# Performance work log

Measured on AMD Instinct MI355X. Metric: run time of the kernel, lower is better.

The kernel has to match this reference:

```python
import jax, jax.numpy as jnp
import numpy as np

DIM = 768
NUM_HEADS = 12
HEAD_DIM = DIM // NUM_HEADS
SCALE = HEAD_DIM ** -0.5


def setup_inputs() -> dict:
    key = jax.random.key(0)
    ks = jax.random.split(key, 6)
    B, N, C = 4, 2048, DIM
    x = jax.random.normal(ks[0], (B, N, C), dtype=jnp.float32)
    qkv_weight = jax.random.normal(ks[1], (3 * C, C), dtype=jnp.float32) * (C ** -0.5)
    q_bias = jax.random.normal(ks[2], (C,), dtype=jnp.float32) * 0.02
    v_bias = jax.random.normal(ks[3], (C,), dtype=jnp.float32) * 0.02
    proj_weight = jax.random.normal(ks[4], (C, C), dtype=jnp.float32) * (C ** -0.5)
    proj_bias = jax.random.normal(ks[5], (C,), dtype=jnp.float32) * 0.02
    return {"x": x, "qkv_weight": qkv_weight, "q_bias": q_bias,
            "v_bias": v_bias, "proj_weight": proj_weight, "proj_bias": proj_bias}


def reference(x, qkv_weight, q_bias, v_bias, proj_weight, proj_bias):
    B, N, C = x.shape
    # bias = concat(q_bias, zeros_like(v_bias), v_bias)
    bias = jnp.concatenate([q_bias, jnp.zeros_like(v_bias), v_bias])
    qkv = x @ qkv_weight.T + bias                      # [B, N, 3C]
    qkv = qkv.reshape(B, N, 3, NUM_HEADS, HEAD_DIM)
    q, k, v = jnp.moveaxis(qkv, 2, 0)                  # each [B, N, H, hd]
    q = jnp.transpose(q, (0, 2, 1, 3)) * SCALE         # [B, H, N, hd]
    k = jnp.transpose(k, (0, 2, 1, 3))
    v = jnp.transpose(v, (0, 2, 1, 3))
    attn = jax.nn.softmax(jnp.einsum('bhqd,bhkd->bhqk', q, k), axis=-1)
    out = jnp.einsum('bhqk,bhkd->bhqd', attn, v)       # [B, H, N, hd]
    out = jnp.transpose(out, (0, 2, 1, 3)).reshape(B, N, C)
    return out @ proj_weight.T + proj_bias
```

## Files before the change

kernel.cpp:

```cpp
#include <hip/hip_runtime.h>
#include <cstdint>
#include <cstddef>

typedef _Float16 f16;
typedef _Float16 f16x8 __attribute__((ext_vector_type(8)));
typedef _Float16 f16x4 __attribute__((ext_vector_type(4)));
typedef __fp16 h16x2 __attribute__((ext_vector_type(2)));
typedef float f32x4 __attribute__((ext_vector_type(4)));

#define DIM 768
#define NHEAD 12
#define HD 64
#define BATCH 4
#define SEQ 2048
#define MROWS (BATCH*SEQ)
#define C3 (3*DIM)
#define NBH (BATCH*NHEAD)

__device__ __forceinline__ f32x4 mfma32(f16x8 a, f16x8 b, f32x4 c) {
  return __builtin_amdgcn_mfma_f32_16x16x32_f16(a, b, c, 0, 0, 0);
}
__device__ __forceinline__ f32x4 mfma16(f16x4 a, f16x4 b, f32x4 c) {
  return __builtin_amdgcn_mfma_f32_16x16x16f16(a, b, c, 0, 0, 0);
}

__device__ __forceinline__ void gl2lds16(const void* g, void* l) {
  __builtin_amdgcn_global_load_lds(
      (const __attribute__((address_space(1))) void*)g,
      (__attribute__((address_space(3))) void*)l, 16, 0, 0);
}

__global__ __launch_bounds__(256) void k_convert(
    const float* __restrict__ x, const float* __restrict__ wqkv,
    const float* __restrict__ wproj,
    f16* __restrict__ xh, f16* __restrict__ wqh, f16* __restrict__ wph)
{
  const int NX = MROWS*DIM/4, NW = C3*DIM/4;
  int i = blockIdx.x * 256 + threadIdx.x;
  const float4* src; f16* dst; int idx;
  if (i < NX)         { src = (const float4*)x;     dst = xh;  idx = i; }
  else if (i < NX+NW) { src = (const float4*)wqkv;  dst = wqh; idx = i - NX; }
  else                { src = (const float4*)wproj; dst = wph; idx = i - NX - NW; }
  float4 v = src[idx];
  union { f16 h[4]; uint64_t u; } r;
  r.h[0] = (f16)v.x; r.h[1] = (f16)v.y; r.h[2] = (f16)v.z; r.h[3] = (f16)v.w;
  ((uint64_t*)dst)[idx] = r.u;
}

__device__ __forceinline__ void gemm_tile(
    const f16* __restrict__ A, const f16* __restrict__ B,
    int lda, int ldb, int K, int am0, int bn0,
    f16* smem, f32x4 acc[4][4])
{
  f16* sA0 = smem;         f16* sA1 = smem + 4096;
  f16* sB0 = smem + 8192;  f16* sB1 = smem + 12288;
  const int tid = threadIdx.x, wid = tid >> 6;
  const int lane = tid & 63, lane15 = lane & 15, quad = lane >> 4;
  const int wm = wid >> 1, wn = wid & 1;

  auto stage = [&](int k0, f16* sA, f16* sB) {
    #pragma unroll
    for (int i = 0; i < 2; i++) {
      int j = i*256 + tid;
      int row = j >> 2;
      int sc  = (j & 3) ^ ((row >> 1) & 3);
      gl2lds16(A + (size_t)(am0 + row)*lda + k0 + sc*8, sA + (i*256 + wid*64)*8);
      gl2lds16(B + (size_t)(bn0 + row)*ldb + k0 + sc*8, sB + (i*256 + wid*64)*8);
    }
  };

  const int NK = K >> 5;
  stage(0, sA0, sB0);
  for (int kk = 0; kk < NK; kk++) {
    f16* cA = (kk & 1) ? sA1 : sA0;
    f16* cB = (kk & 1) ? sB1 : sB0;
    __syncthreads();
    if (kk + 1 < NK)
      stage((kk + 1) << 5, (kk & 1) ? sA0 : sA1, (kk & 1) ? sB0 : sB1);
    f16x8 af[4], bf[4];
    #pragma unroll
    for (int t = 0; t < 4; t++) {
      int ra = wm*64 + t*16 + lane15;
      af[t] = *(const f16x8*)(cA + ra*32 + ((quad ^ ((ra >> 1) & 3)) << 3));
      int rb = wn*64 + t*16 + lane15;
      bf[t] = *(const f16x8*)(cB + rb*32 + ((quad ^ ((rb >> 1) & 3)) << 3));
    }
    #pragma unroll
    for (int mt = 0; mt < 4; mt++)
      #pragma unroll
      for (int nt = 0; nt < 4; nt++)
        acc[mt][nt] = mfma32(af[mt], bf[nt], acc[mt][nt]);
  }
}

__global__ __launch_bounds__(256, 4) void k_qkv(
    const f16* __restrict__ xh, const f16* __restrict__ wqh,
    const float* __restrict__ q_bias, const float* __restrict__ v_bias,
    f16* __restrict__ Qh, f16* __restrict__ Kh, f16* __restrict__ Vt)
{
  __shared__ f16 smem[16384];
  f32x4 acc[4][4];
  const f32x4 z4 = {0.f, 0.f, 0.f, 0.f};
  #pragma unroll
  for (int a = 0; a < 4; a++)
    #pragma unroll
    for (int b = 0; b < 4; b++) acc[a][b] = z4;

  const int tid = threadIdx.x, wid = tid >> 6, lane = tid & 63;
  const int lane15 = lane & 15, quad = lane >> 4;
  const int wm = wid >> 1, wn = wid & 1;
  const int cblk = blockIdx.x * 128;
  const int mblk = blockIdx.y * 128;
  const int bb = mblk >> 11, nbase = mblk & (SEQ - 1);
  const float QS = 0.125f * 1.4426950408889634f;

  if (cblk < 2*DIM) {
    gemm_tile(wqh, xh, DIM, DIM, DIM, cblk, mblk, smem, acc);
    const bool isQ = (cblk < DIM);
    #pragma unroll
    for (int mt = 0; mt < 4; mt++) {
      int c0 = cblk + wm*64 + mt*16 + quad*4;
      int cr = isQ ? c0 : (c0 - DIM);
      int h = cr >> 6, d0 = cr & 63;
      float4 qb4 = isQ ? *(const float4*)(q_bias + c0) : make_float4(0,0,0,0);
      f16* dst = isQ ? Qh : Kh;
      f16* base = dst + (((size_t)(bb*NHEAD + h)*SEQ + nbase) << 6) + d0;
      #pragma unroll
      for (int nt = 0; nt < 4; nt++) {
        int n = wn*64 + nt*16 + lane15;
        f32x4 v = acc[mt][nt];
        f16x4 hv;
        if (isQ) {
          hv[0] = (f16)((v[0] + qb4.x) * QS); hv[1] = (f16)((v[1] + qb4.y) * QS);
          hv[2] = (f16)((v[2] + qb4.z) * QS); hv[3] = (f16)((v[3] + qb4.w) * QS);
        } else {
          hv[0] = (f16)v[0]; hv[1] = (f16)v[1]; hv[2] = (f16)v[2]; hv[3] = (f16)v[3];
        }
        *(f16x4*)(base + ((size_t)n << 6)) = hv;
      }
    }
  } else {
    gemm_tile(xh, wqh, DIM, DIM, DIM, mblk, cblk, smem, acc);
    #pragma unroll
    for (int nt = 0; nt < 4; nt++) {
      int c = cblk + wn*64 + nt*16 + lane15;
      int c2 = c - 2*DIM;
      int h = c2 >> 6, d = c2 & 63;
      float b = v_bias[c2];
      f16* base = Vt + ((size_t)(bb*NHEAD + h)*HD + d)*SEQ + nbase;
      #pragma unroll
      for (int mt = 0; mt < 4; mt++) {
        int n0 = wm*64 + mt*16 + quad*4;
        f32x4 v = acc[mt][nt];
        f16x4 hv = {(f16)(v[0]+b), (f16)(v[1]+b), (f16)(v[2]+b), (f16)(v[3]+b)};
        *(f16x4*)(base + n0) = hv;
      }
    }
  }
}

#define KVT 128
#define NIT (SEQ/KVT)
__global__ __launch_bounds__(256, 3) void k_attn(
    const f16* __restrict__ Qh, const f16* __restrict__ Kh,
    const f16* __restrict__ Vt, f16* __restrict__ attnh)
{
  __shared__ f16 smem[2*8192 + 64*132];
  f16* sK0 = smem;
  f16* sK1 = smem + 8192;
  f16* sV  = smem + 16384;

  const int tid = threadIdx.x, wid = tid >> 6, lane = tid & 63;
  const int lane15 = lane & 15, quad = lane >> 4;
  const int q0 = blockIdx.x * 128;
  const int bh = blockIdx.y;
  const int qw = q0 + wid*32;

  const f16* Kbh = Kh + (size_t)bh*SEQ*HD;
  const f16* Vbh = Vt + (size_t)bh*HD*SEQ;

  f16x8 qf[2][2];
  #pragma unroll
  for (int qt = 0; qt < 2; qt++)
    #pragma unroll
    for (int ks = 0; ks < 2; ks++)
      qf[qt][ks] = *(const f16x8*)(Qh + ((size_t)bh*SEQ + qw + qt*16 + lane15)*HD
                                      + ks*32 + quad*8);

  f32x4 o[4][2];
  f32x4 sacc[2];
  const f32x4 z4 = {0.f, 0.f, 0.f, 0.f};
  #pragma unroll
  for (int dt = 0; dt < 4; dt++)
    #pragma unroll
    for (int qt = 0; qt < 2; qt++) o[dt][qt] = z4;
  sacc[0] = z4; sacc[1] = z4;
  const f16x4 one4 = {(f16)1.f, (f16)1.f, (f16)1.f, (f16)1.f};

  const int vrow = tid >> 2, vcg = (tid & 3) * 32;
  const f16* vsrc = Vbh + (size_t)vrow*SEQ + vcg;

  auto stageK = [&](int kv0, f16* sK) {
    #pragma unroll
    for (int i = 0; i < 4; i++) {
      int j = i*256 + tid;
      int row = j >> 3;
      int sc  = (j & 7) ^ (row & 7);
      gl2lds16(Kbh + (size_t)(kv0 + row)*HD + sc*8, sK + (i*256 + wid*64)*8);
    }
  };

  stageK(0, sK0);
  f16x8 vreg[4];
  #pragma unroll
  for (int j = 0; j < 4; j++) vreg[j] = *(const f16x8*)(vsrc + j*8);

  for (int it = 0; it < NIT; it++) {
    f16* cK = (it & 1) ? sK1 : sK0;
    __syncthreads();
    #pragma unroll
    for (int j = 0; j < 4; j++) {
      union { f16x8 v; f16x4 h[2]; } u; u.v = vreg[j];
      *(f16x4*)(sV + vrow*132 + vcg + j*8)     = u.h[0];
      *(f16x4*)(sV + vrow*132 + vcg + j*8 + 4) = u.h[1];
    }
    __syncthreads();
    if (it + 1 < NIT) {
      stageK((it + 1)*KVT, (it & 1) ? sK0 : sK1);
      #pragma unroll
      for (int j = 0; j < 4; j++)
        vreg[j] = *(const f16x8*)(vsrc + (it + 1)*KVT + j*8);
    }

    #pragma unroll
    for (int c = 0; c < 4; c++) {
      f16x8 ka[2][2];
      #pragma unroll
      for (int kt = 0; kt < 2; kt++) {
        int rb = c*32 + kt*16 + lane15;
        #pragma unroll
        for (int ks = 0; ks < 2; ks++)
          ka[ks][kt] = *(const f16x8*)(cK + rb*64 + (((ks*4 + quad) ^ (rb & 7)) << 3));
      }
      f32x4 s[2][2];
      #pragma unroll
      for (int kt = 0; kt < 2; kt++)
        #pragma unroll
        for (int qt = 0; qt < 2; qt++) s[kt][qt] = z4;
      #pragma unroll
      for (int ks = 0; ks < 2; ks++)
        #pragma unroll
        for (int kt = 0; kt < 2; kt++)
          #pragma unroll
          for (int qt = 0; qt < 2; qt++)
            s[kt][qt] = mfma32(ka[ks][kt], qf[qt][ks], s[kt][qt]);

      f16x4 pb[2][2];
      #pragma unroll
      for (int kt = 0; kt < 2; kt++)
        #pragma unroll
        for (int qt = 0; qt < 2; qt++) {
          union { h16x2 g2[2]; f16x4 h4; } u;
          u.g2[0] = __builtin_amdgcn_cvt_pkrtz(exp2f(s[kt][qt][0]), exp2f(s[kt][qt][1]));
          u.g2[1] = __builtin_amdgcn_cvt_pkrtz(exp2f(s[kt][qt][2]), exp2f(s[kt][qt][3]));
          pb[kt][qt] = u.h4;
        }
      #pragma unroll
      for (int kt = 0; kt < 2; kt++)
        #pragma unroll
        for (int qt = 0; qt < 2; qt++)
          sacc[qt] = mfma16(one4, pb[kt][qt], sacc[qt]);

      #pragma unroll
      for (int dt = 0; dt < 4; dt++) {
        int row = dt*16 + lane15;
        #pragma unroll
        for (int kt = 0; kt < 2; kt++) {
          int c16 = 4*c + 2*kt + (quad >> 1);
          f16x4 va = *(const f16x4*)(sV + row*132 + c16*8 + (quad & 1)*4);
          #pragma unroll
          for (int qt = 0; qt < 2; qt++)
            o[dt][qt] = mfma16(va, pb[kt][qt], o[dt][qt]);
        }
      }
    }
  }

  float inv[2] = {1.f / sacc[0][0], 1.f / sacc[1][0]};

  __syncthreads();
  f16* tb = smem + wid * (32 * 72);
  #pragma unroll
  for (int dt = 0; dt < 4; dt++)
    #pragma unroll
    for (int qt = 0; qt < 2; qt++) {
      f32x4 v = o[dt][qt];
      float iv = inv[qt];
      f16x4 hx = {(f16)(v[0]*iv), (f16)(v[1]*iv), (f16)(v[2]*iv), (f16)(v[3]*iv)};
      *(f16x4*)(tb + (qt*16 + lane15)*72 + dt*16 + quad*4) = hx;
    }
  __syncthreads();
  const int b = bh / NHEAD, h = bh % NHEAD;
  #pragma unroll
  for (int i = 0; i < 4; i++) {
    int row = i*8 + (lane >> 3);
    f16x8 rv = *(const f16x8*)(tb + row*72 + (lane & 7)*8);
    *(f16x8*)(attnh + ((size_t)b*SEQ + qw + row)*DIM + h*HD + (lane & 7)*8) = rv;
  }
}

__global__ __launch_bounds__(256, 4) void k_proj(
    const f16* __restrict__ ah, const f16* __restrict__ wph,
    const float* __restrict__ pbias, float* __restrict__ out)
{
  __shared__ f16 smem[16384];
  f32x4 acc[4][4];
  const f32x4 z4 = {0.f, 0.f, 0.f, 0.f};
  #pragma unroll
  for (int a = 0; a < 4; a++)
    #pragma unroll
    for (int b = 0; b < 4; b++) acc[a][b] = z4;

  const int cblk = blockIdx.y * 128;
  const int mblk = blockIdx.x * 128;
  gemm_tile(wph, ah, DIM, DIM, DIM, cblk, mblk, smem, acc);

  const int tid = threadIdx.x, wid = tid >> 6, lane = tid & 63;
  const int lane15 = lane & 15, quad = lane >> 4;
  const int wm = wid >> 1, wn = wid & 1;
  #pragma unroll
  for (int mt = 0; mt < 4; mt++) {
    int c0 = cblk + wm*64 + mt*16 + quad*4;
    float4 b4 = *(const float4*)(pbias + c0);
    #pragma unroll
    for (int nt = 0; nt < 4; nt++) {
      int m = mblk + wn*64 + nt*16 + lane15;
      f32x4 v = acc[mt][nt];
      float4 r = make_float4(v[0]+b4.x, v[1]+b4.y, v[2]+b4.z, v[3]+b4.w);
      *(float4*)(out + (size_t)m*DIM + c0) = r;
    }
  }
}

extern "C" void kernel_launch(void* const* d_in, const int* in_sizes, int n_in,
                              void* d_out, int out_size, void* d_ws, size_t ws_size,
                              hipStream_t stream) {
  const float* x    = (const float*)d_in[0];
  const float* wqkv = (const float*)d_in[1];
  const float* qb   = (const float*)d_in[2];
  const float* vb   = (const float*)d_in[3];
  const float* wp   = (const float*)d_in[4];
  const float* pb   = (const float*)d_in[5];
  float* out = (float*)d_out;

  f16* p = (f16*)d_ws;
  f16* xh  = p; p += (size_t)MROWS*DIM;
  f16* wqh = p; p += (size_t)C3*DIM;
  f16* wph = p; p += (size_t)DIM*DIM;
  f16* Qh  = p; p += (size_t)NBH*SEQ*HD;
  f16* Kh  = p; p += (size_t)NBH*SEQ*HD;
  f16* Vt  = p; p += (size_t)NBH*SEQ*HD;
  f16* attnh = xh;

  k_convert<<<8448, 256, 0, stream>>>(x, wqkv, wp, xh, wqh, wph);
  k_qkv<<<dim3(C3/128, MROWS/128), 256, 0, stream>>>(xh, wqh, qb, vb, Qh, Kh, Vt);
  k_attn<<<dim3(SEQ/128, NBH), 256, 0, stream>>>(Qh, Kh, Vt, attnh);
  k_proj<<<dim3(MROWS/128, DIM/128), 256, 0, stream>>>(attnh, wph, pb, out);
}
```

Measured before the change: 235.5 us.

## Use 2-wave attention blocks with 64 queries per wave; shrink proj tile to 128x64

```diff
diff --git a/kernel.cpp b/kernel.cpp
--- a/kernel.cpp
+++ b/kernel.cpp
@@ -89,6 +89,57 @@
     for (int mt = 0; mt < 4; mt++)
       #pragma unroll
       for (int nt = 0; nt < 4; nt++)
+        acc[mt][nt] = mfma32(af[mt], bf[nt], acc[mt][nt]);
+  }
+}
+
+__device__ __forceinline__ void gemm_tile_128x64(
+    const f16* __restrict__ A, const f16* __restrict__ B,
+    int lda, int ldb, int K, int am0, int bn0,
+    f16* smem, f32x4 acc[4][2])
+{
+  f16* sA0 = smem;         f16* sA1 = smem + 4096;
+  f16* sB0 = smem + 8192;  f16* sB1 = smem + 10240;
+  const int tid = threadIdx.x, wid = tid >> 6;
+  const int lane = tid & 63, lane15 = lane & 15, quad = lane >> 4;
+  const int wm = wid >> 1, wn = wid & 1;
+
+  auto stage = [&](int k0, f16* sA, f16* sB) {
+    #pragma unroll
+    for (int i = 0; i < 2; i++) {
+      int j = i*256 + tid;
+      int row = j >> 2;
+      int sc  = (j & 3) ^ ((row >> 1) & 3);
+      gl2lds16(A + (size_t)(am0 + row)*lda + k0 + sc*8, sA + (i*256 + wid*64)*8);
+    }
+    int rowb = tid >> 2;
+    int scb  = (tid & 3) ^ ((rowb >> 1) & 3);
+    gl2lds16(B + (size_t)(bn0 + rowb)*ldb + k0 + scb*8, sB + (wid*64)*8);
+  };
+
+  const int NK = K >> 5;
+  stage(0, sA0, sB0);
+  for (int kk = 0; kk < NK; kk++) {
+    f16* cA = (kk & 1) ? sA1 : sA0;
+    f16* cB = (kk & 1) ? sB1 : sB0;
+    __syncthreads();
+    if (kk + 1 < NK)
+      stage((kk + 1) << 5, (kk & 1) ? sA0 : sA1, (kk & 1) ? sB0 : sB1);
+    f16x8 af[4], bf[2];
+    #pragma unroll
+    for (int t = 0; t < 4; t++) {
+      int ra = wm*64 + t*16 + lane15;
+      af[t] = *(const f16x8*)(cA + ra*32 + ((quad ^ ((ra >> 1) & 3)) << 3));
+    }
+    #pragma unroll
+    for (int t = 0; t < 2; t++) {
+      int rb = wn*32 + t*16 + lane15;
+      bf[t] = *(const f16x8*)(cB + rb*32 + ((quad ^ ((rb >> 1) & 3)) << 3));
+    }
+    #pragma unroll
+    for (int mt = 0; mt < 4; mt++)
+      #pragma unroll
+      for (int nt = 0; nt < 2; nt++)
         acc[mt][nt] = mfma32(af[mt], bf[nt], acc[mt][nt]);
   }
 }
@@ -161,7 +212,7 @@
 
 #define KVT 128
 #define NIT (SEQ/KVT)
-__global__ __launch_bounds__(256, 3) void k_attn(
+__global__ __launch_bounds__(128, 2) void k_attn(
     const f16* __restrict__ Qh, const f16* __restrict__ Kh,
     const f16* __restrict__ Vt, f16* __restrict__ attnh)
 {
@@ -174,52 +225,53 @@
   const int lane15 = lane & 15, quad = lane >> 4;
   const int q0 = blockIdx.x * 128;
   const int bh = blockIdx.y;
-  const int qw = q0 + wid*32;
+  const int qw = q0 + wid*64;
 
   const f16* Kbh = Kh + (size_t)bh*SEQ*HD;
   const f16* Vbh = Vt + (size_t)bh*HD*SEQ;
 
-  f16x8 qf[2][2];
-  #pragma unroll
-  for (int qt = 0; qt < 2; qt++)
+  f16x8 qf[4][2];
+  #pragma unroll
+  for (int qt = 0; qt < 4; qt++)
     #pragma unroll
     for (int ks = 0; ks < 2; ks++)
       qf[qt][ks] = *(const f16x8*)(Qh + ((size_t)bh*SEQ + qw + qt*16 + lane15)*HD
                                       + ks*32 + quad*8);
 
-  f32x4 o[4][2];
-  f32x4 sacc[2];
+  f32x4 o[4][4];
+  f32x4 sacc[4];
   const f32x4 z4 = {0.f, 0.f, 0.f, 0.f};
   #pragma unroll
   for (int dt = 0; dt < 4; dt++)
     #pragma unroll
-    for (int qt = 0; qt < 2; qt++) o[dt][qt] = z4;
-  sacc[0] = z4; sacc[1] = z4;
+    for (int qt = 0; qt < 4; qt++) o[dt][qt] = z4;
+  #pragma unroll
+  for (int qt = 0; qt < 4; qt++) sacc[qt] = z4;
   const f16x4 one4 = {(f16)1.f, (f16)1.f, (f16)1.f, (f16)1.f};
 
-  const int vrow = tid >> 2, vcg = (tid & 3) * 32;
+  const int vrow = tid >> 1, vcg = (tid & 1) * 64;
   const f16* vsrc = Vbh + (size_t)vrow*SEQ + vcg;
 
   auto stageK = [&](int kv0, f16* sK) {
     #pragma unroll
-    for (int i = 0; i < 4; i++) {
-      int j = i*256 + tid;
+    for (int i = 0; i < 8; i++) {
+      int j = i*128 + tid;
       int row = j >> 3;
       int sc  = (j & 7) ^ (row & 7);
-      gl2lds16(Kbh + (size_t)(kv0 + row)*HD + sc*8, sK + (i*256 + wid*64)*8);
+      gl2lds16(Kbh + (size_t)(kv0 + row)*HD + sc*8, sK + (i*128 + wid*64)*8);
     }
   };
 
   stageK(0, sK0);
-  f16x8 vreg[4];
-  #pragma unroll
-  for (int j = 0; j < 4; j++) vreg[j] = *(const f16x8*)(vsrc + j*8);
+  f16x8 vreg[8];
+  #pragma unroll
+  for (int j = 0; j < 8; j++) vreg[j] = *(const f16x8*)(vsrc + j*8);
 
   for (int it = 0; it < NIT; it++) {
     f16* cK = (it & 1) ? sK1 : sK0;
     __syncthreads();
     #pragma unroll
-    for (int j = 0; j < 4; j++) {
+    for (int j = 0; j < 8; j++) {
       union { f16x8 v; f16x4 h[2]; } u; u.v = vreg[j];
       *(f16x4*)(sV + vrow*132 + vcg + j*8)     = u.h[0];
       *(f16x4*)(sV + vrow*132 + vcg + j*8 + 4) = u.h[1];
@@ -228,7 +280,7 @@
     if (it + 1 < NIT) {
       stageK((it + 1)*KVT, (it & 1) ? sK0 : sK1);
       #pragma unroll
-      for (int j = 0; j < 4; j++)
+      for (int j = 0; j < 8; j++)
         vreg[j] = *(const f16x8*)(vsrc + (it + 1)*KVT + j*8);
     }
 
@@ -242,24 +294,24 @@
         for (int ks = 0; ks < 2; ks++)
           ka[ks][kt] = *(const f16x8*)(cK + rb*64 + (((ks*4 + quad) ^ (rb & 7)) << 3));
       }
-      f32x4 s[2][2];
+      f32x4 s[2][4];
       #pragma unroll
       for (int kt = 0; kt < 2; kt++)
         #pragma unroll
-        for (int qt = 0; qt < 2; qt++) s[kt][qt] = z4;
+        for (int qt = 0; qt < 4; qt++) s[kt][qt] = z4;
       #pragma unroll
       for (int ks = 0; ks < 2; ks++)
         #pragma unroll
         for (int kt = 0; kt < 2; kt++)
           #pragma unroll
-          for (int qt = 0; qt < 2; qt++)
+          for (int qt = 0; qt < 4; qt++)
             s[kt][qt] = mfma32(ka[ks][kt], qf[qt][ks], s[kt][qt]);
 
-      f16x4 pb[2][2];
+      f16x4 pb[2][4];
       #pragma unroll
       for (int kt = 0; kt < 2; kt++)
         #pragma unroll
-        for (int qt = 0; qt < 2; qt++) {
+        for (int qt = 0; qt < 4; qt++) {
           union { h16x2 g2[2]; f16x4 h4; } u;
           u.g2[0] = __builtin_amdgcn_cvt_pkrtz(exp2f(s[kt][qt][0]), exp2f(s[kt][qt][1]));
           u.g2[1] = __builtin_amdgcn_cvt_pkrtz(exp2f(s[kt][qt][2]), exp2f(s[kt][qt][3]));
@@ -268,7 +320,7 @@
       #pragma unroll
       for (int kt = 0; kt < 2; kt++)
         #pragma unroll
-        for (int qt = 0; qt < 2; qt++)
+        for (int qt = 0; qt < 4; qt++)
           sacc[qt] = mfma16(one4, pb[kt][qt], sacc[qt]);
 
       #pragma unroll
@@ -279,51 +331,52 @@
           int c16 = 4*c + 2*kt + (quad >> 1);
           f16x4 va = *(const f16x4*)(sV + row*132 + c16*8 + (quad & 1)*4);
           #pragma unroll
-          for (int qt = 0; qt < 2; qt++)
+          for (int qt = 0; qt < 4; qt++)
             o[dt][qt] = mfma16(va, pb[kt][qt], o[dt][qt]);
         }
       }
     }
   }
 
-  float inv[2] = {1.f / sacc[0][0], 1.f / sacc[1][0]};
+  float inv[4];
+  #pragma unroll
+  for (int qt = 0; qt < 4; qt++) inv[qt] = 1.f / sacc[qt][0];
 
   __syncthreads();
-  f16* tb = smem + wid * (32 * 72);
+  f16* tb = smem + wid * (64 * 72);
   #pragma unroll
   for (int dt = 0; dt < 4; dt++)
     #pragma unroll
-    for (int qt = 0; qt < 2; qt++) {
+    for (int qt = 0; qt < 4; qt++) {
       f32x4 v = o[dt][qt];
       float iv = inv[qt];
       f16x4 hx = {(f16)(v[0]*iv), (f16)(v[1]*iv), (f16)(v[2]*iv), (f16)(v[3]*iv)};
       *(f16x4*)(tb + (qt*16 + lane15)*72 + dt*16 + quad*4) = hx;
     }
-  __syncthreads();
   const int b = bh / NHEAD, h = bh % NHEAD;
   #pragma unroll
-  for (int i = 0; i < 4; i++) {
+  for (int i = 0; i < 8; i++) {
     int row = i*8 + (lane >> 3);
     f16x8 rv = *(const f16x8*)(tb + row*72 + (lane & 7)*8);
     *(f16x8*)(attnh + ((size_t)b*SEQ + qw + row)*DIM + h*HD + (lane & 7)*8) = rv;
   }
 }
 
-__global__ __launch_bounds__(256, 4) void k_proj(
+__global__ __launch_bounds__(256, 3) void k_proj(
     const f16* __restrict__ ah, const f16* __restrict__ wph,
     const float* __restrict__ pbias, float* __restrict__ out)
 {
-  __shared__ f16 smem[16384];
-  f32x4 acc[4][4];
+  __shared__ f16 smem[12288];
+  f32x4 acc[4][2];
   const f32x4 z4 = {0.f, 0.f, 0.f, 0.f};
   #pragma unroll
   for (int a = 0; a < 4; a++)
     #pragma unroll
-    for (int b = 0; b < 4; b++) acc[a][b] = z4;
+    for (int b = 0; b < 2; b++) acc[a][b] = z4;
 
   const int cblk = blockIdx.y * 128;
-  const int mblk = blockIdx.x * 128;
-  gemm_tile(wph, ah, DIM, DIM, DIM, cblk, mblk, smem, acc);
+  const int mblk = blockIdx.x * 64;
+  gemm_tile_128x64(wph, ah, DIM, DIM, DIM, cblk, mblk, smem, acc);
 
   const int tid = threadIdx.x, wid = tid >> 6, lane = tid & 63;
   const int lane15 = lane & 15, quad = lane >> 4;
@@ -333,8 +386,8 @@
     int c0 = cblk + wm*64 + mt*16 + quad*4;
     float4 b4 = *(const float4*)(pbias + c0);
     #pragma unroll
-    for (int nt = 0; nt < 4; nt++) {
-      int m = mblk + wn*64 + nt*16 + lane15;
+    for (int nt = 0; nt < 2; nt++) {
+      int m = mblk + wn*32 + nt*16 + lane15;
       f32x4 v = acc[mt][nt];
       float4 r = make_float4(v[0]+b4.x, v[1]+b4.y, v[2]+b4.z, v[3]+b4.w);
       *(float4*)(out + (size_t)m*DIM + c0) = r;
@@ -364,6 +417,6 @@
 
   k_convert<<<8448, 256, 0, stream>>>(x, wqkv, wp, xh, wqh, wph);
   k_qkv<<<dim3(C3/128, MROWS/128), 256, 0, stream>>>(xh, wqh, qb, vb, Qh, Kh, Vt);
-  k_attn<<<dim3(SEQ/128, NBH), 256, 0, stream>>>(Qh, Kh, Vt, attnh);
-  k_proj<<<dim3(MROWS/128, DIM/128), 256, 0, stream>>>(attnh, wph, pb, out);
-}
+  k_attn<<<dim3(SEQ/128, NBH), 128, 0, stream>>>(Qh, Kh, Vt, attnh);
+  k_proj<<<dim3(MROWS/64, DIM/128), 256, 0, stream>>>(attnh, wph, pb, out);
+}
```

New measurement: 265.2 us. 12.6% more time.

## Replace LDS-staged GEMM with direct global-to-register fragment loads and smaller tiles

Applied to the files above, without the earlier changes.

```diff
diff --git a/kernel.cpp b/kernel.cpp
--- a/kernel.cpp
+++ b/kernel.cpp
@@ -47,49 +47,45 @@
   ((uint64_t*)dst)[idx] = r.u;
 }
 
-__device__ __forceinline__ void gemm_tile(
+template<int MT, int NT>
+__device__ __forceinline__ void gemm_g(
     const f16* __restrict__ A, const f16* __restrict__ B,
-    int lda, int ldb, int K, int am0, int bn0,
-    f16* smem, f32x4 acc[4][4])
-{
-  f16* sA0 = smem;         f16* sA1 = smem + 4096;
-  f16* sB0 = smem + 8192;  f16* sB1 = smem + 12288;
+    int am0, int bn0, f32x4 acc[MT][NT])
+{
   const int tid = threadIdx.x, wid = tid >> 6;
   const int lane = tid & 63, lane15 = lane & 15, quad = lane >> 4;
   const int wm = wid >> 1, wn = wid & 1;
-
-  auto stage = [&](int k0, f16* sA, f16* sB) {
-    #pragma unroll
-    for (int i = 0; i < 2; i++) {
-      int j = i*256 + tid;
-      int row = j >> 2;
-      int sc  = (j & 3) ^ ((row >> 1) & 3);
-      gl2lds16(A + (size_t)(am0 + row)*lda + k0 + sc*8, sA + (i*256 + wid*64)*8);
-      gl2lds16(B + (size_t)(bn0 + row)*ldb + k0 + sc*8, sB + (i*256 + wid*64)*8);
-    }
-  };
-
-  const int NK = K >> 5;
-  stage(0, sA0, sB0);
-  for (int kk = 0; kk < NK; kk++) {
-    f16* cA = (kk & 1) ? sA1 : sA0;
-    f16* cB = (kk & 1) ? sB1 : sB0;
-    __syncthreads();
-    if (kk + 1 < NK)
-      stage((kk + 1) << 5, (kk & 1) ? sA0 : sA1, (kk & 1) ? sB0 : sB1);
-    f16x8 af[4], bf[4];
-    #pragma unroll
-    for (int t = 0; t < 4; t++) {
-      int ra = wm*64 + t*16 + lane15;
-      af[t] = *(const f16x8*)(cA + ra*32 + ((quad ^ ((ra >> 1) & 3)) << 3));
-      int rb = wn*64 + t*16 + lane15;
-      bf[t] = *(const f16x8*)(cB + rb*32 + ((quad ^ ((rb >> 1) & 3)) << 3));
-    }
-    #pragma unroll
-    for (int mt = 0; mt < 4; mt++)
-      #pragma unroll
-      for (int nt = 0; nt < 4; nt++)
-        acc[mt][nt] = mfma32(af[mt], bf[nt], acc[mt][nt]);
+  const f16* pa = A + (size_t)(am0 + wm*(MT*16) + lane15)*DIM + quad*8;
+  const f16* pb = B + (size_t)(bn0 + wn*(NT*16) + lane15)*DIM + quad*8;
+
+  f16x8 aF[2][MT], bF[2][NT];
+  #pragma unroll
+  for (int t = 0; t < MT; t++) aF[0][t] = *(const f16x8*)(pa + t*16*DIM);
+  #pragma unroll
+  for (int t = 0; t < NT; t++) bF[0][t] = *(const f16x8*)(pb + t*16*DIM);
+
+  #pragma unroll
+  for (int kk = 0; kk < 24; kk += 2) {
+    #pragma unroll
+    for (int t = 0; t < MT; t++) aF[1][t] = *(const f16x8*)(pa + t*16*DIM + (kk+1)*32);
+    #pragma unroll
+    for (int t = 0; t < NT; t++) bF[1][t] = *(const f16x8*)(pb + t*16*DIM + (kk+1)*32);
+    #pragma unroll
+    for (int mt = 0; mt < MT; mt++)
+      #pragma unroll
+      for (int nt = 0; nt < NT; nt++)
+        acc[mt][nt] = mfma32(aF[0][mt], bF[0][nt], acc[mt][nt]);
+    if (kk + 2 < 24) {
+      #pragma unroll
+      for (int t = 0; t < MT; t++) aF[0][t] = *(const f16x8*)(pa + t*16*DIM + (kk+2)*32);
+      #pragma unroll
+      for (int t = 0; t < NT; t++) bF[0][t] = *(const f16x8*)(pb + t*16*DIM + (kk+2)*32);
+    }
+    #pragma unroll
+    for (int mt = 0; mt < MT; mt++)
+      #pragma unroll
+      for (int nt = 0; nt < NT; nt++)
+        acc[mt][nt] = mfma32(aF[1][mt], bF[1][nt], acc[mt][nt]);
   }
 }
 
@@ -98,24 +94,24 @@
     const float* __restrict__ q_bias, const float* __restrict__ v_bias,
     f16* __restrict__ Qh, f16* __restrict__ Kh, f16* __restrict__ Vt)
 {
-  __shared__ f16 smem[16384];
-  f32x4 acc[4][4];
-  const f32x4 z4 = {0.f, 0.f, 0.f, 0.f};
-  #pragma unroll
-  for (int a = 0; a < 4; a++)
-    #pragma unroll
-    for (int b = 0; b < 4; b++) acc[a][b] = z4;
-
   const int tid = threadIdx.x, wid = tid >> 6, lane = tid & 63;
   const int lane15 = lane & 15, quad = lane >> 4;
   const int wm = wid >> 1, wn = wid & 1;
-  const int cblk = blockIdx.x * 128;
-  const int mblk = blockIdx.y * 128;
-  const int bb = mblk >> 11, nbase = mblk & (SEQ - 1);
+  const int id = blockIdx.x;
   const float QS = 0.125f * 1.4426950408889634f;
 
-  if (cblk < 2*DIM) {
-    gemm_tile(wqh, xh, DIM, DIM, DIM, cblk, mblk, smem, acc);
+  f32x4 acc[4][2];
+  const f32x4 z4 = {0.f, 0.f, 0.f, 0.f};
+  #pragma unroll
+  for (int a = 0; a < 4; a++)
+    #pragma unroll
+    for (int b = 0; b < 2; b++) acc[a][b] = z4;
+
+  if (id < 1536) {
+    const int cblk = (id % 12) * 128;
+    const int mblk = (id / 12) * 64;
+    gemm_g<4,2>(wqh, xh, cblk, mblk, acc);
+    const int bb = mblk >> 11, nbase = mblk & (SEQ - 1);
     const bool isQ = (cblk < DIM);
     #pragma unroll
     for (int mt = 0; mt < 4; mt++) {
@@ -126,8 +122,8 @@
       f16* dst = isQ ? Qh : Kh;
       f16* base = dst + (((size_t)(bb*NHEAD + h)*SEQ + nbase) << 6) + d0;
       #pragma unroll
-      for (int nt = 0; nt < 4; nt++) {
-        int n = wn*64 + nt*16 + lane15;
+      for (int nt = 0; nt < 2; nt++) {
+        int n = wn*32 + nt*16 + lane15;
         f32x4 v = acc[mt][nt];
         f16x4 hv;
         if (isQ) {
@@ -140,10 +136,14 @@
       }
     }
   } else {
-    gemm_tile(xh, wqh, DIM, DIM, DIM, mblk, cblk, smem, acc);
-    #pragma unroll
-    for (int nt = 0; nt < 4; nt++) {
-      int c = cblk + wn*64 + nt*16 + lane15;
+    const int vid = id - 1536;
+    const int mblk = (vid % 64) * 128;
+    const int cblk = 2*DIM + (vid / 64) * 64;
+    gemm_g<4,2>(xh, wqh, mblk, cblk, acc);
+    const int bb = mblk >> 11, nbase = mblk & (SEQ - 1);
+    #pragma unroll
+    for (int nt = 0; nt < 2; nt++) {
+      int c = cblk + wn*32 + nt*16 + lane15;
       int c2 = c - 2*DIM;
       int h = c2 >> 6, d = c2 & 63;
       float b = v_bias[c2];
@@ -313,24 +313,25 @@
     const f16* __restrict__ ah, const f16* __restrict__ wph,
     const float* __restrict__ pbias, float* __restrict__ out)
 {
-  __shared__ f16 smem[16384];
-  f32x4 acc[4][4];
-  const f32x4 z4 = {0.f, 0.f, 0.f, 0.f};
-  #pragma unroll
-  for (int a = 0; a < 4; a++)
-    #pragma unroll
-    for (int b = 0; b < 4; b++) acc[a][b] = z4;
-
-  const int cblk = blockIdx.y * 128;
-  const int mblk = blockIdx.x * 128;
-  gemm_tile(wph, ah, DIM, DIM, DIM, cblk, mblk, smem, acc);
-
   const int tid = threadIdx.x, wid = tid >> 6, lane = tid & 63;
   const int lane15 = lane & 15, quad = lane >> 4;
   const int wm = wid >> 1, wn = wid & 1;
-  #pragma unroll
-  for (int mt = 0; mt < 4; mt++) {
-    int c0 = cblk + wm*64 + mt*16 + quad*4;
+  const int id = blockIdx.x;
+  const int cblk = (id % 12) * 64;
+  const int mblk = (id / 12) * 128;
+
+  f32x4 acc[2][4];
+  const f32x4 z4 = {0.f, 0.f, 0.f, 0.f};
+  #pragma unroll
+  for (int a = 0; a < 2; a++)
+    #pragma unroll
+    for (int b = 0; b < 4; b++) acc[a][b] = z4;
+
+  gemm_g<2,4>(wph, ah, cblk, mblk, acc);
+
+  #pragma unroll
+  for (int mt = 0; mt < 2; mt++) {
+    int c0 = cblk + wm*32 + mt*16 + quad*4;
     float4 b4 = *(const float4*)(pbias + c0);
     #pragma unroll
     for (int nt = 0; nt < 4; nt++) {
@@ -363,7 +364,7 @@
   f16* attnh = xh;
 
   k_convert<<<8448, 256, 0, stream>>>(x, wqkv, wp, xh, wqh, wph);
-  k_qkv<<<dim3(C3/128, MROWS/128), 256, 0, stream>>>(xh, wqh, qb, vb, Qh, Kh, Vt);
+  k_qkv<<<2304, 256, 0, stream>>>(xh, wqh, qb, vb, Qh, Kh, Vt);
   k_attn<<<dim3(SEQ/128, NBH), 256, 0, stream>>>(Qh, Kh, Vt, attnh);
-  k_proj<<<dim3(MROWS/128, DIM/128), 256, 0, stream>>>(attnh, wph, pb, out);
-}
+  k_proj<<<768, 256, 0, stream>>>(attnh, wph, pb, out);
+}
```

After: 381.4 us. 1.62x slower.
